# Kernel tuning notes

Measured on AMD Instinct MI355X. Metric: run time of the kernel, lower is better.

The kernel has to match this reference:

```python
import jax, jax.numpy as jnp
import numpy as np

NPOINT = 1024
NSAMPLE = 32
EPS = 1e-5


def setup_inputs() -> dict:
    key = jax.random.key(0)
    ks = jax.random.split(key, 8)
    B, N, D = 16, 4096, 64
    xyz = jax.random.normal(ks[0], (B, N, 3), dtype=jnp.float32)
    points = jax.random.normal(ks[1], (B, N, D), dtype=jnp.float32)

    def mk(k, o, i):
        return (jax.random.normal(k, (o, i), dtype=jnp.float32) * 0.05,
                jnp.zeros((o,), jnp.float32),   # conv bias
                jnp.ones((o,), jnp.float32),    # bn gamma
                jnp.zeros((o,), jnp.float32))   # bn beta

    W0, b0, g0, be0 = mk(ks[2], 64, 67)
    W1, b1, g1, be1 = mk(ks[3], 64, 64)
    W2, b2, g2, be2 = mk(ks[4], 128, 64)
    return dict(xyz=xyz, points=points,
                W0=W0, b0=b0, g0=g0, be0=be0,
                W1=W1, b1=b1, g1=g1, be1=be1,
                W2=W2, b2=b2, g2=g2, be2=be2)


def _fps(xyz, npoint):
    # Sequential farthest point sampling. xyz: [B,N,3] -> idx [B,npoint] int32.
    B, N, _ = xyz.shape
    bidx = jnp.arange(B)

    def step(carry, _):
        distance, farthest = carry
        centroid = xyz[bidx, farthest][:, None, :]          # [B,1,3]
        d = jnp.sum((xyz - centroid) ** 2, -1)              # [B,N]
        distance = jnp.minimum(distance, d)
        new_far = jnp.argmax(distance, -1).astype(jnp.int32)
        return (distance, new_far), farthest

    init = (jnp.full((B, N), jnp.inf, dtype=xyz.dtype),
            jnp.full((B,), N // 2, dtype=jnp.int32))
    _, cents = jax.lax.scan(step, init, None, length=npoint)
    return cents.T                                          # [B, npoint]


def _gather(p, idx):
    # p: [B,N,C], idx: [B,...] -> [B,...,C]
    return jax.vmap(lambda a, i: a[i])(p, idx)


def reference(xyz, points, W0, b0, g0, be0, W1, b1, g1, be1, W2, b2, g2, be2):
    B, N, _ = xyz.shape
    fps_idx = _fps(xyz, NPOINT)                             # [B,M]
    new_xyz = _gather(xyz, fps_idx)                         # [B,M,3]

    # squared distances [B,M,N], then k smallest neighbors
    d = (jnp.sum(new_xyz ** 2, -1)[:, :, None]
         + jnp.sum(xyz ** 2, -1)[:, None, :]
         - 2.0 * jnp.einsum('bmc,bnc->bmn', new_xyz, xyz))
    _, idx = jax.lax.top_k(-d, NSAMPLE)                     # [B,M,K]

    grouped_xyz = _gather(xyz, idx)                         # [B,M,K,3]
    rel = grouped_xyz - new_xyz[:, :, None, :]
    grouped_feat = _gather(points, idx)                     # [B,M,K,D]
    g = jnp.concatenate([rel, grouped_feat], axis=-1)       # [B,M,K,3+D]

    # 1x1 conv + BatchNorm2d (training-mode batch stats) + ReLU
    for W, b, gm, bt in ((W0, b0, g0, be0), (W1, b1, g1, be1), (W2, b2, g2, be2)):
        x = jnp.einsum('bmkc,oc->bmko', g, W) + b
        mu = x.mean((0, 1, 2))
        var = x.var((0, 1, 2))
        g = jax.nn.relu(gm * (x - mu) * jax.lax.rsqrt(var + EPS) + bt)

    new_points = g.max(axis=2)                              # [B,M,C_out]
    return new_xyz, new_points, fps_idx
```

## Files before the change

### kernel.cpp

```cpp
#include <hip/hip_runtime.h>
#include <math.h>

#define B_ 16
#define N_ 4096
#define D_ 64
#define M_ 1024
#define K_ 32
#define RTOT (B_*M_*K_)
#define EPSF 1e-5f

#define WT0B_OFF  0
#define WT1B_OFF  3072
#define WT2B_OFF  5120
#define ST_OFF    9216
#define BN_OFF    9728
#define NXW_OFF   10240
#define KIDX_OFF  59392
#define PK_OFF    583680
#define Y0B_OFF   2680832
#define PTS4_OFF  Y0B_OFF
#define Y1B_OFF   19458048
#define SB0_OFF   36235264
#define SB1_OFF   (SB0_OFF + 8192)
#define SB2_OFF   (SB1_OFF + 8192)
#define WS_FAST_BYTES ((unsigned long long)(SB2_OFF + 16384) * 4ull)

typedef __attribute__((ext_vector_type(8))) short bf16x8;
typedef __attribute__((ext_vector_type(4))) float f32x4;

__device__ inline unsigned bf16u(float x) {
    unsigned u = __float_as_uint(x);
    return (u + 0x7FFFu + ((u >> 16) & 1u)) >> 16;
}
__device__ inline float ubf(unsigned short h) {
    return __uint_as_float(((unsigned)h) << 16);
}

__global__ void prep_kernel(const float* __restrict__ W0, const float* __restrict__ W1,
                            const float* __restrict__ W2, float* __restrict__ ws,
                            int zero_sb) {
    int tid = threadIdx.x;
    if (blockIdx.x > 0) {
        if (zero_sb) {
            float* sb = ws + SB0_OFF + (blockIdx.x - 1) * 2048;
            for (int i = tid; i < 2048; i += 256) sb[i] = 0.f;
        }
        return;
    }
    unsigned short* wt0b = (unsigned short*)(ws + WT0B_OFF);
    unsigned short* wt1b = (unsigned short*)(ws + WT1B_OFF);
    unsigned short* wt2b = (unsigned short*)(ws + WT2B_OFF);
    float* st = ws + ST_OFF;
    for (int i = tid; i < 512; i += 256) st[i] = 0.f;
    for (int i = tid; i < 64*96; i += 256) {
        int o = i / 96, k = i - o*96;
        float w = 0.f;
        if (k < 64)      w = W0[o*67 + 3 + k];
        else if (k < 67) w = W0[o*67 + (k - 64)];
        wt0b[i] = (unsigned short)bf16u(w);
    }
    for (int i = tid; i < 64*64; i += 256)  wt1b[i] = (unsigned short)bf16u(W1[i]);
    for (int i = tid; i < 128*64; i += 256) wt2b[i] = (unsigned short)bf16u(W2[i]);
}

__global__ __launch_bounds__(256) void fps_kernel(const float* __restrict__ xyz,
                                                  float* __restrict__ out_newxyz,
                                                  float* __restrict__ out_fpsidx,
                                                  float* __restrict__ ws_newxyz,
                                                  float4* __restrict__ pts4g) {
#pragma clang fp contract(off)
    __shared__ float4 pts[N_];
    __shared__ int selidx[M_];
    __shared__ __align__(32) unsigned long long red[2][4];
    const int b = blockIdx.x;
    const int tid = threadIdx.x;
    const int lane = tid & 63, wave = tid >> 6;
    const float* xb = xyz + (size_t)b * N_ * 3;
    for (int i = tid; i < N_; i += 256) {
        float x = xb[i*3+0], y = xb[i*3+1], z = xb[i*3+2];
        pts[i] = make_float4(x, y, z, 0.f);
        if (pts4g) {
            float pp = x*x + y*y; pp = pp + z*z;
            pts4g[b*N_ + i] = make_float4(x, y, z, pp);
        }
    }
    __syncthreads();
    float px[16], py[16], pz[16], dist[16];
#pragma unroll
    for (int j = 0; j < 16; ++j) {
        float4 p = pts[(tid << 4) + j];
        px[j] = p.x; py[j] = p.y; pz[j] = p.z;
        dist[j] = 3.4e38f;
    }
    int cur = N_/2;
    for (int t = 0; t < M_; ++t) {
        if (tid == (t & 255)) selidx[t] = cur;
        if (t == M_-1) break;
        float4 c4 = pts[cur];
        float cx = c4.x, cy = c4.y, cz = c4.z;
        float bm0 = -1.f, bm1 = -1.f, bm2 = -1.f, bm3 = -1.f;
        int bj0 = 0, bj1 = 4, bj2 = 8, bj3 = 12;
#pragma unroll
        for (int j = 0; j < 4; ++j) {
            {
                float dx = px[j]-cx, dy = py[j]-cy, dz = pz[j]-cz;
                float a = dx*dx, b2 = dy*dy, c2 = dz*dz;
                float d = (a + b2) + c2;
                float nd = fminf(dist[j], d); dist[j] = nd;
                bool bt = nd > bm0; bm0 = bt ? nd : bm0; bj0 = bt ? j : bj0;
            }
            {
                int k = j + 4;
                float dx = px[k]-cx, dy = py[k]-cy, dz = pz[k]-cz;
                float a = dx*dx, b2 = dy*dy, c2 = dz*dz;
                float d = (a + b2) + c2;
                float nd = fminf(dist[k], d); dist[k] = nd;
                bool bt = nd > bm1; bm1 = bt ? nd : bm1; bj1 = bt ? k : bj1;
            }
            {
                int k = j + 8;
                float dx = px[k]-cx, dy = py[k]-cy, dz = pz[k]-cz;
                float a = dx*dx, b2 = dy*dy, c2 = dz*dz;
                float d = (a + b2) + c2;
                float nd = fminf(dist[k], d); dist[k] = nd;
                bool bt = nd > bm2; bm2 = bt ? nd : bm2; bj2 = bt ? k : bj2;
            }
            {
                int k = j + 12;
                float dx = px[k]-cx, dy = py[k]-cy, dz = pz[k]-cz;
                float a = dx*dx, b2 = dy*dy, c2 = dz*dz;
                float d = (a + b2) + c2;
                float nd = fminf(dist[k], d); dist[k] = nd;
                bool bt = nd > bm3; bm3 = bt ? nd : bm3; bj3 = bt ? k : bj3;
            }
        }
        float bv = bm0; int bj = bj0;
        if (bm1 > bv) { bv = bm1; bj = bj1; }
        if (bm2 > bv) { bv = bm2; bj = bj2; }
        if (bm3 > bv) { bv = bm3; bj = bj3; }
        unsigned mybits = __float_as_uint(bv);
        unsigned vr = mybits;
        { unsigned o = (unsigned)__builtin_amdgcn_update_dpp((int)vr,(int)vr,0x121,0xF,0xF,false); if (o > vr) vr = o; }
        { unsigned o = (unsigned)__builtin_amdgcn_update_dpp((int)vr,(int)vr,0x122,0xF,0xF,false); if (o > vr) vr = o; }
        { unsigned o = (unsigned)__builtin_amdgcn_update_dpp((int)vr,(int)vr,0x124,0xF,0xF,false); if (o > vr) vr = o; }
        { unsigned o = (unsigned)__builtin_amdgcn_update_dpp((int)vr,(int)vr,0x128,0xF,0xF,false); if (o > vr) vr = o; }
        unsigned r0 = (unsigned)__builtin_amdgcn_readlane((int)vr, 0);
        unsigned r1 = (unsigned)__builtin_amdgcn_readlane((int)vr, 16);
        unsigned r2 = (unsigned)__builtin_amdgcn_readlane((int)vr, 32);
        unsigned r3 = (unsigned)__builtin_amdgcn_readlane((int)vr, 48);
        unsigned m01 = (r0 > r1) ? r0 : r1;
        unsigned m23 = (r2 > r3) ? r2 : r3;
        unsigned vmax = (m01 > m23) ? m01 : m23;
        unsigned long long mask = __ballot(mybits == vmax);
        int wl = (int)__builtin_ctzll(mask);
        int gidx = (tid << 4) + bj;
        int sel = __builtin_amdgcn_readlane(gidx, wl);
        unsigned long long key = ((unsigned long long)vmax << 32) | (unsigned)(~sel);
        int buf = t & 1;
        if (lane == 0) red[buf][wave] = key;
        __syncthreads();
        unsigned long long k0 = red[buf][0], k1 = red[buf][1];
        unsigned long long k2 = red[buf][2], k3 = red[buf][3];
        unsigned long long km01 = (k0 > k1) ? k0 : k1;
        unsigned long long km23 = (k2 > k3) ? k2 : k3;
        unsigned long long km   = (km01 > km23) ? km01 : km23;
        cur = (int)((~(unsigned)km) & (N_-1));
    }
    __syncthreads();
    for (int i = tid; i < M_; i += 256) {
        int c = selidx[i];
        out_fpsidx[b*M_ + i] = (float)c;
        float4 p = pts[c];
        size_t o3 = (size_t)(b*M_ + i)*3;
        out_newxyz[o3+0] = p.x; out_newxyz[o3+1] = p.y; out_newxyz[o3+2] = p.z;
        ws_newxyz[o3+0] = p.x;  ws_newxyz[o3+1] = p.y;  ws_newxyz[o3+2] = p.z;
    }
}

__global__ __launch_bounds__(256) void knn_kernel4(const float4* __restrict__ pts4,
                                                   const float* __restrict__ ws_newxyz,
                                                   int* __restrict__ knn_idx) {
#pragma clang fp contract(off)
    const int lane = threadIdx.x & 63;
    const int q = blockIdx.x * 4 + (threadIdx.x >> 6);
    const int b = q >> 10;
    const float4* pb = pts4 + (size_t)b * N_;
    float qx = ws_newxyz[q*3+0], qy = ws_newxyz[q*3+1], qz = ws_newxyz[q*3+2];
    float qq = qx*qx + qy*qy; qq = qq + qz*qz;
    float val[64];
    float m1 = 3.4e38f, m2 = 3.4e38f; int k1 = 0, k2 = 0;
#pragma unroll
    for (int k = 0; k < 64; ++k) {
        float4 p = pb[(k<<6) + lane];
        float dot = qx*p.x + qy*p.y; dot = dot + qz*p.z;
        float d = (qq + p.w) - 2.0f*dot;
        val[k] = d;
        bool lt1 = d < m1, lt2 = d < m2;
        k2 = lt1 ? k1 : (lt2 ? k : k2);
        m2 = fminf(fmaxf(d, m1), m2);
        k1 = lt1 ? k : k1;
        m1 = fminf(d, m1);
    }
    unsigned long long consumed = 0ull;
    bool has2 = true;
    unsigned int myOut = 0;
    for (int r = 0; r < 32; ++r) {
        unsigned int u = __float_as_uint(m1);
        u = (u & 0x80000000u) ? ~u : (u | 0x80000000u);
        unsigned long long pk = ((unsigned long long)u << 32) | (unsigned)(lane + (k1<<6));
#pragma unroll
        for (int off = 32; off > 0; off >>= 1) {
            unsigned long long o = __shfl_xor(pk, off);
            pk = (o < pk) ? o : pk;
        }
        unsigned g = (unsigned)pk;
        if (lane == r) myOut = g;
        if (lane == (int)(g & 63u)) {
            consumed |= (1ull << k1);
            if (has2) { m1 = m2; k1 = k2; has2 = false; }
            else {
                m1 = 3.4e38f; k1 = 0;
#pragma unroll
                for (int k = 0; k < 64; ++k) {
                    bool ok = !((consumed >> k) & 1ull) && (val[k] < m1);
                    m1 = ok ? val[k] : m1;
                    k1 = ok ? k : k1;
                }
            }
        }
    }
    if (lane < 32) knn_idx[q*32 + lane] = (int)myOut;
}

__global__ __launch_bounds__(256) void knn_kernel(const float* __restrict__ xyz,
                                                  const float* __restrict__ ws_newxyz,
                                                  int* __restrict__ knn_idx) {
#pragma clang fp contract(off)
    const int lane = threadIdx.x & 63;
    const int q = blockIdx.x * 4 + (threadIdx.x >> 6);
    const int b = q >> 10;
    const float* xb = xyz + (size_t)b * N_ * 3;
    float qx = ws_newxyz[q*3+0], qy = ws_newxyz[q*3+1], qz = ws_newxyz[q*3+2];
    float qq = qx*qx + qy*qy; qq = qq + qz*qz;
    float val[64];
    float m1 = 3.4e38f, m2 = 3.4e38f; int k1 = 0, k2 = 0;
#pragma unroll
    for (int k = 0; k < 64; ++k) {
        int n = (k<<6) + lane;
        float x = xb[n*3+0], y = xb[n*3+1], z = xb[n*3+2];
        float pp = x*x + y*y; pp = pp + z*z;
        float dot = qx*x + qy*y; dot = dot + qz*z;
        float d = (qq + pp) - 2.0f*dot;
        val[k] = d;
        if (d < m1)      { m2 = m1; k2 = k1; m1 = d; k1 = k; }
        else if (d < m2) { m2 = d; k2 = k; }
    }
    unsigned long long consumed = 0ull;
    bool has2 = true;
    unsigned int myOut = 0;
    for (int r = 0; r < 32; ++r) {
        unsigned int u = __float_as_uint(m1);
        u = (u & 0x80000000u) ? ~u : (u | 0x80000000u);
        unsigned long long pk = ((unsigned long long)u << 32) | (unsigned)(lane + (k1<<6));
#pragma unroll
        for (int off = 32; off > 0; off >>= 1) {
            unsigned long long o = __shfl_xor(pk, off);
            pk = (o < pk) ? o : pk;
        }
        unsigned g = (unsigned)pk;
        if (lane == r) myOut = g;
        if (lane == (int)(g & 63u)) {
            consumed |= (1ull << k1);
            if (has2) { m1 = m2; k1 = k2; has2 = false; }
            else {
                m1 = 3.4e38f; k1 = 0;
#pragma unroll
                for (int k = 0; k < 64; ++k) {
                    bool ok = !((consumed >> k) & 1ull) && (val[k] < m1);
                    m1 = ok ? val[k] : m1;
                    k1 = ok ? k : k1;
                }
            }
        }
    }
    if (lane < 32) knn_idx[q*32 + lane] = (int)myOut;
}

__global__ __launch_bounds__(256) void pass0_kernel(
    const float* __restrict__ xyz, const float* __restrict__ points,
    const float* __restrict__ nxw, const int* __restrict__ kidx,
    const unsigned short* __restrict__ wt0b, const float* __restrict__ cb0,
    float* __restrict__ sb,
    unsigned short* __restrict__ y0b)
{
    __shared__ __align__(16) unsigned short XsB[64*104];
    __shared__ __align__(16) unsigned short W0B[64*104];
    __shared__ int sidx[64];
    __shared__ float sAcc[64], qAcc[64];
    const int tid = threadIdx.x;
    const int r0 = blockIdx.x * 64;
    const int lane = tid & 63, wv = tid >> 6;
    const int mrow = lane & 15, quad = lane >> 4;

    if (tid < 64) { sidx[tid] = kidx[r0 + tid]; sAcc[tid] = 0.f; qAcc[tid] = 0.f; }
    {
        const uint4* s = (const uint4*)wt0b;
        for (int i = tid; i < 768; i += 256) {
            int r = i / 12, ch = i - r*12;
            *(uint4*)(W0B + r*104 + ch*8) = s[i];
        }
    }
    __syncthreads();

    {
        int row = tid >> 2, q4 = tid & 3;
        int gr = r0 + row;
        int qq = gr >> 5, bb = qq >> 10;
        int n = sidx[row];
        const float4* src = (const float4*)(points + ((size_t)(bb*N_ + n))*64 + q4*16);
        float4 f0 = src[0], f1 = src[1], f2 = src[2], f3 = src[3];
        uint4 u0, u1;
        u0.x = bf16u(f0.x) | (bf16u(f0.y) << 16);
        u0.y = bf16u(f0.z) | (bf16u(f0.w) << 16);
        u0.z = bf16u(f1.x) | (bf16u(f1.y) << 16);
        u0.w = bf16u(f1.z) | (bf16u(f1.w) << 16);
        u1.x = bf16u(f2.x) | (bf16u(f2.y) << 16);
        u1.y = bf16u(f2.z) | (bf16u(f2.w) << 16);
        u1.z = bf16u(f3.x) | (bf16u(f3.y) << 16);
        u1.w = bf16u(f3.z) | (bf16u(f3.w) << 16);
        *(uint4*)(XsB + row*104 + q4*16)     = u0;
        *(uint4*)(XsB + row*104 + q4*16 + 8) = u1;
        uint4 z;
        if (q4 == 0) {
            float rx = xyz[((size_t)(bb*N_ + n))*3 + 0] - nxw[qq*3 + 0];
            float ry = xyz[((size_t)(bb*N_ + n))*3 + 1] - nxw[qq*3 + 1];
            float rz = xyz[((size_t)(bb*N_ + n))*3 + 2] - nxw[qq*3 + 2];
            z.x = bf16u(rx) | (bf16u(ry) << 16);
            z.y = bf16u(rz);
            z.z = 0; z.w = 0;
        } else { z.x = 0; z.y = 0; z.z = 0; z.w = 0; }
        *(uint4*)(XsB + row*104 + 64 + q4*8) = z;
    }
    __syncthreads();

    const int arow = wv*16 + mrow;
    f32x4 acc0[4];
#pragma unroll
    for (int ct = 0; ct < 4; ++ct) {
        float bv = cb0[ct*16 + mrow];
        acc0[ct] = (f32x4){bv, bv, bv, bv};
    }
#pragma unroll
    for (int kk = 0; kk < 96; kk += 32) {
        bf16x8 a = *(const bf16x8*)(XsB + arow*104 + kk + quad*8);
#pragma unroll
        for (int ct = 0; ct < 4; ++ct) {
            bf16x8 b = *(const bf16x8*)(W0B + (ct*16 + mrow)*104 + kk + quad*8);
            acc0[ct] = __builtin_amdgcn_mfma_f32_16x16x32_bf16(a, b, acc0[ct], 0, 0, 0);
        }
    }
#pragma unroll
    for (int ct = 0; ct < 4; ++ct) {
        f32x4 v = acc0[ct];
        float s = (v.x + v.y) + (v.z + v.w);
        float q = (v.x*v.x + v.y*v.y) + (v.z*v.z + v.w*v.w);
        atomicAdd(&sAcc[ct*16 + mrow], s);
        atomicAdd(&qAcc[ct*16 + mrow], q);
    }
    __syncthreads();
    unsigned short* STG = W0B;
    const int rbase = wv*16 + quad*4;
#pragma unroll
    for (int ct = 0; ct < 4; ++ct) {
        int col = ct*16 + mrow;
        f32x4 v = acc0[ct];
        STG[(rbase+0)*72 + col] = (unsigned short)bf16u(v.x);
        STG[(rbase+1)*72 + col] = (unsigned short)bf16u(v.y);
        STG[(rbase+2)*72 + col] = (unsigned short)bf16u(v.z);
        STG[(rbase+3)*72 + col] = (unsigned short)bf16u(v.w);
    }
    __syncthreads();
    for (int i = tid; i < 512; i += 256) {
        int r = i >> 3, c8 = i & 7;
        *(uint4*)(y0b + (size_t)(r0 + r)*64 + c8*8) = *(const uint4*)(STG + r*72 + c8*8);
    }
    int bk = blockIdx.x & 63;
    if (tid < 64) {
        atomicAdd(sb + bk*64 + tid, sAcc[tid]);
        atomicAdd(sb + 4096 + bk*64 + tid, qAcc[tid]);
    }
}

__global__ __launch_bounds__(256) void pass1_kernel(
    const unsigned short* __restrict__ y0b, const unsigned short* __restrict__ wt1b,
    const float* __restrict__ cb1, const float* __restrict__ bnab0,
    float* __restrict__ sb,
    unsigned short* __restrict__ y1b)
{
    __shared__ __align__(16) unsigned short W1B[64*72];
    __shared__ __align__(16) unsigned short STG[64*72];
    __shared__ float sAcc[64], qAcc[64];
    const int tid = threadIdx.x;
    const int r0 = blockIdx.x * 64;
    const int lane = tid & 63, wv = tid >> 6;
    const int mrow = lane & 15, quad = lane >> 4;

    {
        const uint4* s = (const uint4*)wt1b;
        for (int i = tid; i < 512; i += 256) {
            int r = i >> 3, ch = i & 7;
            *(uint4*)(W1B + r*72 + ch*8) = s[i];
        }
    }
    if (tid < 64) { sAcc[tid] = 0.f; qAcc[tid] = 0.f; }

    const int gr = r0 + wv*16 + mrow;
    bf16x8 raw0 = *(const bf16x8*)(y0b + (size_t)gr*64 + quad*8);
    bf16x8 raw1 = *(const bf16x8*)(y0b + (size_t)gr*64 + 32 + quad*8);
    bf16x8 a0, a1;
    {
        const float* A = bnab0 + quad*8;
        const float* S = bnab0 + 64 + quad*8;
#pragma unroll
        for (int j = 0; j < 8; ++j) {
            float f = ubf((unsigned short)raw0[j]);
            a0[j] = (short)bf16u(fmaxf(fmaf(A[j], f, S[j]), 0.f));
        }
        const float* A2 = bnab0 + 32 + quad*8;
        const float* S2 = bnab0 + 96 + quad*8;
#pragma unroll
        for (int j = 0; j < 8; ++j) {
            float f = ubf((unsigned short)raw1[j]);
            a1[j] = (short)bf16u(fmaxf(fmaf(A2[j], f, S2[j]), 0.f));
        }
    }
    __syncthreads();

    f32x4 acc[4];
#pragma unroll
    for (int ct = 0; ct < 4; ++ct) {
        float bv = cb1[ct*16 + mrow];
        acc[ct] = (f32x4){bv, bv, bv, bv};
    }
#pragma unroll
    for (int ct = 0; ct < 4; ++ct) {
        bf16x8 b0 = *(const bf16x8*)(W1B + (ct*16 + mrow)*72 + quad*8);
        bf16x8 b1 = *(const bf16x8*)(W1B + (ct*16 + mrow)*72 + 32 + quad*8);
        acc[ct] = __builtin_amdgcn_mfma_f32_16x16x32_bf16(a0, b0, acc[ct], 0, 0, 0);
        acc[ct] = __builtin_amdgcn_mfma_f32_16x16x32_bf16(a1, b1, acc[ct], 0, 0, 0);
    }
#pragma unroll
    for (int ct = 0; ct < 4; ++ct) {
        f32x4 v = acc[ct];
        float s = (v.x + v.y) + (v.z + v.w);
        float q = (v.x*v.x + v.y*v.y) + (v.z*v.z + v.w*v.w);
        atomicAdd(&sAcc[ct*16 + mrow], s);
        atomicAdd(&qAcc[ct*16 + mrow], q);
    }
    const int rbase = wv*16 + quad*4;
#pragma unroll
    for (int ct = 0; ct < 4; ++ct) {
        int col = ct*16 + mrow;
        f32x4 v = acc[ct];
        STG[(rbase+0)*72 + col] = (unsigned short)bf16u(v.x);
        STG[(rbase+1)*72 + col] = (unsigned short)bf16u(v.y);
        STG[(rbase+2)*72 + col] = (unsigned short)bf16u(v.z);
        STG[(rbase+3)*72 + col] = (unsigned short)bf16u(v.w);
    }
    __syncthreads();
    for (int i = tid; i < 512; i += 256) {
        int r = i >> 3, c8 = i & 7;
        *(uint4*)(y1b + (size_t)(r0 + r)*64 + c8*8) = *(const uint4*)(STG + r*72 + c8*8);
    }
    int bk = blockIdx.x & 63;
    if (tid < 64) {
        atomicAdd(sb + bk*64 + tid, sAcc[tid]);
        atomicAdd(sb + 4096 + bk*64 + tid, qAcc[tid]);
    }
}

__global__ __launch_bounds__(256) void pass2_kernel(
    const unsigned short* __restrict__ y1b, const unsigned short* __restrict__ wt2b,
    const float* __restrict__ cb2, const float* __restrict__ bnab1,
    float* __restrict__ sb,
    unsigned int* __restrict__ packed)
{
    __shared__ __align__(16) unsigned short W2B[128*72];
    __shared__ float sAcc[128], qAcc[128];
    __shared__ float mxs[4*128], mns[4*128];
    const int tid = threadIdx.x;
    const int r0 = blockIdx.x * 64;
    const int lane = tid & 63, wv = tid >> 6;
    const int mrow = lane & 15, quad = lane >> 4;

    {
        const uint4* s = (const uint4*)wt2b;
        for (int i = tid; i < 1024; i += 256) {
            int r = i >> 3, ch = i & 7;
            *(uint4*)(W2B + r*72 + ch*8) = s[i];
        }
    }
    if (tid < 128) { sAcc[tid] = 0.f; qAcc[tid] = 0.f; }

    const int gr = r0 + wv*16 + mrow;
    bf16x8 raw0 = *(const bf16x8*)(y1b + (size_t)gr*64 + quad*8);
    bf16x8 raw1 = *(const bf16x8*)(y1b + (size_t)gr*64 + 32 + quad*8);
    bf16x8 a0, a1;
    {
        const float* A = bnab1 + quad*8;
        const float* S = bnab1 + 64 + quad*8;
#pragma unroll
        for (int j = 0; j < 8; ++j) {
            float f = ubf((unsigned short)raw0[j]);
            a0[j] = (short)bf16u(fmaxf(fmaf(A[j], f, S[j]), 0.f));
        }
        const float* A2 = bnab1 + 32 + quad*8;
        const float* S2 = bnab1 + 96 + quad*8;
#pragma unroll
        for (int j = 0; j < 8; ++j) {
            float f = ubf((unsigned short)raw1[j]);
            a1[j] = (short)bf16u(fmaxf(fmaf(A2[j], f, S2[j]), 0.f));
        }
    }
    __syncthreads();

    f32x4 acc[8];
#pragma unroll
    for (int ct = 0; ct < 8; ++ct) {
        float bv = cb2[ct*16 + mrow];
        acc[ct] = (f32x4){bv, bv, bv, bv};
    }
#pragma unroll
    for (int ct = 0; ct < 8; ++ct) {
        bf16x8 b0 = *(const bf16x8*)(W2B + (ct*16 + mrow)*72 + quad*8);
        bf16x8 b1 = *(const bf16x8*)(W2B + (ct*16 + mrow)*72 + 32 + quad*8);
        acc[ct] = __builtin_amdgcn_mfma_f32_16x16x32_bf16(a0, b0, acc[ct], 0, 0, 0);
        acc[ct] = __builtin_amdgcn_mfma_f32_16x16x32_bf16(a1, b1, acc[ct], 0, 0, 0);
    }
#pragma unroll
    for (int ct = 0; ct < 8; ++ct) {
        f32x4 v = acc[ct];
        float s = (v.x + v.y) + (v.z + v.w);
        float q = (v.x*v.x + v.y*v.y) + (v.z*v.z + v.w*v.w);
        atomicAdd(&sAcc[ct*16 + mrow], s);
        atomicAdd(&qAcc[ct*16 + mrow], q);
    }
#pragma unroll
    for (int ct = 0; ct < 8; ++ct) {
        f32x4 v = acc[ct];
        float mx = fmaxf(fmaxf(v.x, v.y), fmaxf(v.z, v.w));
        float mn = fminf(fminf(v.x, v.y), fminf(v.z, v.w));
        { float o = __shfl_xor(mx, 16); mx = fmaxf(mx, o); }
        { float o = __shfl_xor(mn, 16); mn = fminf(mn, o); }
        { float o = __shfl_xor(mx, 32); mx = fmaxf(mx, o); }
        { float o = __shfl_xor(mn, 32); mn = fminf(mn, o); }
        if (quad == 0) {
            mxs[wv*128 + ct*16 + mrow] = mx;
            mns[wv*128 + ct*16 + mrow] = mn;
        }
    }
    __syncthreads();
    {
        int g = tid >> 7, c = tid & 127;
        float mx = fmaxf(mxs[(2*g)*128 + c], mxs[(2*g+1)*128 + c]);
        float mn = fminf(mns[(2*g)*128 + c], mns[(2*g+1)*128 + c]);
        packed[(size_t)(blockIdx.x*2 + g)*128 + c] = (bf16u(mx) << 16) | bf16u(mn);
    }
    int bk = blockIdx.x & 63;
    if (tid < 128) {
        atomicAdd(sb + bk*128 + tid, sAcc[tid]);
        atomicAdd(sb + 8192 + bk*128 + tid, qAcc[tid]);
    }
}

template<int DEPTH>
__global__ __launch_bounds__(256) void mlp_pass(
    const float* __restrict__ xyz, const float* __restrict__ points,
    const float* __restrict__ nxw, const int* __restrict__ kidx,
    const unsigned short* __restrict__ wt0b, const unsigned short* __restrict__ wt1b,
    const unsigned short* __restrict__ wt2b,
    const float* __restrict__ cb0, const float* __restrict__ cb1,
    const float* __restrict__ cb2,
    const float* __restrict__ bnab0, const float* __restrict__ bnab1,
    float* __restrict__ statS, float* __restrict__ statQ,
    unsigned int* __restrict__ packed)
{
    __shared__ __align__(16) unsigned short XsB[64*104];
    __shared__ __align__(16) unsigned short W0B[64*104];
    __shared__ __align__(16) unsigned short W1B[(DEPTH>=2) ? 64*72 : 8];
    __shared__ __align__(16) unsigned short W2B[(DEPTH==3) ? 128*72 : 8];
    __shared__ __align__(16) unsigned short Gb [(DEPTH>=2) ? 64*72 : 8];
    __shared__ float sAcc[128], qAcc[128];
    __shared__ float mxs[(DEPTH==3) ? 4*128 : 1];
    __shared__ float mns[(DEPTH==3) ? 4*128 : 1];

    const int tid = threadIdx.x;
    const int r0 = blockIdx.x * 64;
    const int lane = tid & 63, wv = tid >> 6;
    const int mrow = lane & 15, quad = lane >> 4;

    {
        const uint4* s = (const uint4*)wt0b;
        for (int i = tid; i < 768; i += 256) {
            int r = i / 12, ch = i - r*12;
            *(uint4*)(W0B + r*104 + ch*8) = s[i];
        }
    }
    if constexpr (DEPTH >= 2) {
        const uint4* s = (const uint4*)wt1b;
        for (int i = tid; i < 512; i += 256) {
            int r = i >> 3, ch = i & 7;
            *(uint4*)(W1B + r*72 + ch*8) = s[i];
        }
    }
    if constexpr (DEPTH == 3) {
        const uint4* s = (const uint4*)wt2b;
        for (int i = tid; i < 1024; i += 256) {
            int r = i >> 3, ch = i & 7;
            *(uint4*)(W2B + r*72 + ch*8) = s[i];
        }
    }
    if (tid < 128) { sAcc[tid] = 0.f; qAcc[tid] = 0.f; }

    for (int i = tid; i < 64*96; i += 256) {
        int r = i / 96, c = i - r*96;
        int gr = r0 + r;
        int q = gr >> 5;
        int n = kidx[gr];
        int bb = q >> 10;
        float v = 0.f;
        if (c < 64)      v = points[((size_t)(bb*N_ + n))*64 + c];
        else if (c < 67) v = xyz[((size_t)(bb*N_ + n))*3 + (c-64)] - nxw[q*3 + (c-64)];
        XsB[r*104 + c] = (unsigned short)bf16u(v);
    }
    __syncthreads();

    const int arow = wv*16 + mrow;
    f32x4 acc0[4];
#pragma unroll
    for (int ct = 0; ct < 4; ++ct) {
        float bv = cb0[ct*16 + mrow];
        acc0[ct] = (f32x4){bv, bv, bv, bv};
    }
#pragma unroll
    for (int kk = 0; kk < 96; kk += 32) {
        bf16x8 a = *(const bf16x8*)(XsB + arow*104 + kk + quad*8);
#pragma unroll
        for (int ct = 0; ct < 4; ++ct) {
            bf16x8 b = *(const bf16x8*)(W0B + (ct*16 + mrow)*104 + kk + quad*8);
            acc0[ct] = __builtin_amdgcn_mfma_f32_16x16x32_bf16(a, b, acc0[ct], 0, 0, 0);
        }
    }

    if constexpr (DEPTH == 1) {
#pragma unroll
        for (int ct = 0; ct < 4; ++ct) {
            f32x4 v = acc0[ct];
            float s = (v.x + v.y) + (v.z + v.w);
            float q = (v.x*v.x + v.y*v.y) + (v.z*v.z + v.w*v.w);
            atomicAdd(&sAcc[ct*16 + mrow], s);
            atomicAdd(&qAcc[ct*16 + mrow], q);
        }
        __syncthreads();
        if (tid < 64) { atomicAdd(statS + tid, sAcc[tid]); atomicAdd(statQ + tid, qAcc[tid]); }
        return;
    } else {
        const int rbase = wv*16 + quad*4;
#pragma unroll
        for (int ct = 0; ct < 4; ++ct) {
            int col = ct*16 + mrow;
            float a = bnab0[col], sh = bnab0[64 + col];
            f32x4 v = acc0[ct];
            Gb[(rbase+0)*72 + col] = (unsigned short)bf16u(fmaxf(fmaf(a, v.x, sh), 0.f));
            Gb[(rbase+1)*72 + col] = (unsigned short)bf16u(fmaxf(fmaf(a, v.y, sh), 0.f));
            Gb[(rbase+2)*72 + col] = (unsigned short)bf16u(fmaxf(fmaf(a, v.z, sh), 0.f));
            Gb[(rbase+3)*72 + col] = (unsigned short)bf16u(fmaxf(fmaf(a, v.w, sh), 0.f));
        }
        f32x4 acc1[4];
#pragma unroll
        for (int ct = 0; ct < 4; ++ct) {
            float bv = cb1[ct*16 + mrow];
            acc1[ct] = (f32x4){bv, bv, bv, bv};
        }
#pragma unroll
        for (int kk = 0; kk < 64; kk += 32) {
            bf16x8 a = *(const bf16x8*)(Gb + arow*72 + kk + quad*8);
#pragma unroll
            for (int ct = 0; ct < 4; ++ct) {
                bf16x8 b = *(const bf16x8*)(W1B + (ct*16 + mrow)*72 + kk + quad*8);
                acc1[ct] = __builtin_amdgcn_mfma_f32_16x16x32_bf16(a, b, acc1[ct], 0, 0, 0);
            }
        }
        if constexpr (DEPTH == 2) {
#pragma unroll
            for (int ct = 0; ct < 4; ++ct) {
                f32x4 v = acc1[ct];
                float s = (v.x + v.y) + (v.z + v.w);
                float q = (v.x*v.x + v.y*v.y) + (v.z*v.z + v.w*v.w);
                atomicAdd(&sAcc[ct*16 + mrow], s);
                atomicAdd(&qAcc[ct*16 + mrow], q);
            }
            __syncthreads();
            if (tid < 64) { atomicAdd(statS + tid, sAcc[tid]); atomicAdd(statQ + tid, qAcc[tid]); }
            return;
        } else {
#pragma unroll
            for (int ct = 0; ct < 4; ++ct) {
                int col = ct*16 + mrow;
                float a = bnab1[col], sh = bnab1[64 + col];
                f32x4 v = acc1[ct];
                Gb[(rbase+0)*72 + col] = (unsigned short)bf16u(fmaxf(fmaf(a, v.x, sh), 0.f));
                Gb[(rbase+1)*72 + col] = (unsigned short)bf16u(fmaxf(fmaf(a, v.y, sh), 0.f));
                Gb[(rbase+2)*72 + col] = (unsigned short)bf16u(fmaxf(fmaf(a, v.z, sh), 0.f));
                Gb[(rbase+3)*72 + col] = (unsigned short)bf16u(fmaxf(fmaf(a, v.w, sh), 0.f));
            }
            f32x4 acc2[8];
#pragma unroll
            for (int ct = 0; ct < 8; ++ct) {
                float bv = cb2[ct*16 + mrow];
                acc2[ct] = (f32x4){bv, bv, bv, bv};
            }
#pragma unroll
            for (int kk = 0; kk < 64; kk += 32) {
                bf16x8 a = *(const bf16x8*)(Gb + arow*72 + kk + quad*8);
#pragma unroll
                for (int ct = 0; ct < 8; ++ct) {
                    bf16x8 b = *(const bf16x8*)(W2B + (ct*16 + mrow)*72 + kk + quad*8);
                    acc2[ct] = __builtin_amdgcn_mfma_f32_16x16x32_bf16(a, b, acc2[ct], 0, 0, 0);
                }
            }
#pragma unroll
            for (int ct = 0; ct < 8; ++ct) {
                f32x4 v = acc2[ct];
                float s = (v.x + v.y) + (v.z + v.w);
                float q = (v.x*v.x + v.y*v.y) + (v.z*v.z + v.w*v.w);
                atomicAdd(&sAcc[ct*16 + mrow], s);
                atomicAdd(&qAcc[ct*16 + mrow], q);
            }
#pragma unroll
            for (int ct = 0; ct < 8; ++ct) {
                f32x4 v = acc2[ct];
                float mx = fmaxf(fmaxf(v.x, v.y), fmaxf(v.z, v.w));
                float mn = fminf(fminf(v.x, v.y), fminf(v.z, v.w));
                { float o = __shfl_xor(mx, 16); mx = fmaxf(mx, o); }
                { float o = __shfl_xor(mn, 16); mn = fminf(mn, o); }
                { float o = __shfl_xor(mx, 32); mx = fmaxf(mx, o); }
                { float o = __shfl_xor(mn, 32); mn = fminf(mn, o); }
                if (quad == 0) {
                    mxs[wv*128 + ct*16 + mrow] = mx;
                    mns[wv*128 + ct*16 + mrow] = mn;
                }
            }
            __syncthreads();
            {
                int g = tid >> 7, c = tid & 127;
                float mx = fmaxf(mxs[(2*g)*128 + c], mxs[(2*g+1)*128 + c]);
                float mn = fminf(mns[(2*g)*128 + c], mns[(2*g+1)*128 + c]);
                packed[(size_t)(blockIdx.x*2 + g)*128 + c] = (bf16u(mx) << 16) | bf16u(mn);
            }
            if (tid < 128) { atomicAdd(statS + tid, sAcc[tid]); atomicAdd(statQ + tid, qAcc[tid]); }
        }
    }
}

template<int COUT>
__global__ void bn_finalize(const float* __restrict__ stat_s, const float* __restrict__ stat_q,
                            const float* __restrict__ gamma, const float* __restrict__ beta,
                            float* __restrict__ bnab) {
    int c = threadIdx.x;
    if (c < COUT) {
        const float inv_n = 1.f / (float)RTOT;
        float mu  = stat_s[c] * inv_n;
        float var = stat_q[c] * inv_n - mu*mu;
        float inv = 1.f / sqrtf(var + EPSF);
        float a = gamma[c] * inv;
        bnab[c] = a;
        bnab[COUT + c] = beta[c] - mu * a;
    }
}

template<int COUT>
__global__ __launch_bounds__(256) void bn_finalize_bk(const float* __restrict__ sb,
                               const float* __restrict__ gamma, const float* __restrict__ beta,
                               float* __restrict__ bnab) {
    __shared__ float ps[256], pq[256];
    const int tid = threadIdx.x;
    const int c = tid & (COUT - 1);
    const int g = tid / COUT;
    const int G = 256 / COUT;
    const int per = 64 / G;
    float s = 0.f, q = 0.f;
    for (int k = g*per; k < (g+1)*per; ++k) {
        s += sb[k*COUT + c];
        q += sb[64*COUT + k*COUT + c];
    }
    ps[tid] = s; pq[tid] = q;
    __syncthreads();
    if (tid < COUT) {
        for (int g2 = 1; g2 < G; ++g2) { s += ps[g2*COUT + tid]; q += pq[g2*COUT + tid]; }
        const float inv_n = 1.f / (float)RTOT;
        float mu  = s * inv_n;
        float var = q * inv_n - mu*mu;
        float inv = 1.f / sqrtf(var + EPSF);
        float a = gamma[tid] * inv;
        bnab[tid] = a;
        bnab[COUT + tid] = beta[tid] - mu * a;
    }
}

__global__ __launch_bounds__(256) void final_out(const unsigned int* __restrict__ packed,
                                                 const float* __restrict__ bnab2,
                                                 float* __restrict__ out_np) {
    int idx = blockIdx.x*256 + threadIdx.x;
    int c = idx & 127;
    float a = bnab2[c], sh = bnab2[128 + c];
    unsigned p = packed[idx];
    float mx = __uint_as_float(p & 0xFFFF0000u);
    float mn = __uint_as_float(p << 16);
    float x = (a >= 0.f) ? mx : mn;
    out_np[idx] = fmaxf(fmaf(a, x, sh), 0.f);
}

extern "C" void kernel_launch(void* const* d_in, const int* in_sizes, int n_in,
                              void* d_out, int out_size, void* d_ws, size_t ws_size,
                              hipStream_t stream) {
    const float* xyz    = (const float*)d_in[0];
    const float* points = (const float*)d_in[1];
    const float* W0 = (const float*)d_in[2];
    const float* b0 = (const float*)d_in[3];
    const float* g0 = (const float*)d_in[4];
    const float* be0= (const float*)d_in[5];
    const float* W1 = (const float*)d_in[6];
    const float* b1 = (const float*)d_in[7];
    const float* g1 = (const float*)d_in[8];
    const float* be1= (const float*)d_in[9];
    const float* W2 = (const float*)d_in[10];
    const float* b2 = (const float*)d_in[11];
    const float* g2 = (const float*)d_in[12];
    const float* be2= (const float*)d_in[13];

    float* ws  = (float*)d_ws;
    float* out = (float*)d_out;
    float* out_newxyz = out;
    float* out_np     = out + 49152;
    float* out_fpsidx = out + 49152 + 2097152;

    unsigned short* wt0b = (unsigned short*)(ws + WT0B_OFF);
    unsigned short* wt1b = (unsigned short*)(ws + WT1B_OFF);
    unsigned short* wt2b = (unsigned short*)(ws + WT2B_OFF);
    float* s0 = ws + ST_OFF;        float* q0 = s0 + 64;
    float* s1 = q0 + 64;            float* q1 = s1 + 64;
    float* s2 = q1 + 64;            float* q2 = s2 + 128;
    float* bnab0 = ws + BN_OFF;     float* bnab1 = bnab0 + 128;  float* bnab2 = bnab1 + 128;
    float* nxw   = ws + NXW_OFF;
    int*   kidx  = (int*)(ws + KIDX_OFF);
    unsigned int* packed = (unsigned int*)(ws + PK_OFF);
    unsigned short* y0b = (unsigned short*)(ws + Y0B_OFF);
    unsigned short* y1b = (unsigned short*)(ws + Y1B_OFF);
    float4* pts4 = (float4*)(ws + PTS4_OFF);
    float* sb0 = ws + SB0_OFF;
    float* sb1 = ws + SB1_OFF;
    float* sb2 = ws + SB2_OFF;

    int fast = (ws_size >= WS_FAST_BYTES) ? 1 : 0;

    prep_kernel<<<17, 256, 0, stream>>>(W0, W1, W2, ws, fast);
    fps_kernel<<<B_, 256, 0, stream>>>(xyz, out_newxyz, out_fpsidx, nxw,
                                       fast ? pts4 : nullptr);
    if (fast)
        knn_kernel4<<<(B_*M_)/4, 256, 0, stream>>>(pts4, nxw, kidx);
    else
        knn_kernel<<<(B_*M_)/4, 256, 0, stream>>>(xyz, nxw, kidx);

    if (fast) {
        pass0_kernel<<<RTOT/64, 256, 0, stream>>>(xyz, points, nxw, kidx, wt0b, b0, sb0, y0b);
        bn_finalize_bk<64><<<1, 256, 0, stream>>>(sb0, g0, be0, bnab0);
        pass1_kernel<<<RTOT/64, 256, 0, stream>>>(y0b, wt1b, b1, bnab0, sb1, y1b);
        bn_finalize_bk<64><<<1, 256, 0, stream>>>(sb1, g1, be1, bnab1);
        pass2_kernel<<<RTOT/64, 256, 0, stream>>>(y1b, wt2b, b2, bnab1, sb2, packed);
        bn_finalize_bk<128><<<1, 256, 0, stream>>>(sb2, g2, be2, bnab2);
    } else {
        mlp_pass<1><<<RTOT/64, 256, 0, stream>>>(xyz, points, nxw, kidx, wt0b, wt1b, wt2b,
            b0, b1, b2, nullptr, nullptr, s0, q0, nullptr);
        bn_finalize<64><<<1, 64, 0, stream>>>(s0, q0, g0, be0, bnab0);
        mlp_pass<2><<<RTOT/64, 256, 0, stream>>>(xyz, points, nxw, kidx, wt0b, wt1b, wt2b,
            b0, b1, b2, bnab0, nullptr, s1, q1, nullptr);
        bn_finalize<64><<<1, 64, 0, stream>>>(s1, q1, g1, be1, bnab1);
        mlp_pass<3><<<RTOT/64, 256, 0, stream>>>(xyz, points, nxw, kidx, wt0b, wt1b, wt2b,
            b0, b1, b2, bnab0, bnab1, s2, q2, packed);
        bn_finalize<128><<<1, 128, 0, stream>>>(s2, q2, g2, be2, bnab2);
    }

    final_out<<<(B_*M_*128)/256, 256, 0, stream>>>(packed, bnab2, out_np);
}
```

Measured before the change: 1.309 ms.

## Recompute layer-1 in pass2, pre-convert points to bf16, DPP reduction in kNN

pass1 now only accumulates BatchNorm statistics and no longer writes y1 to global memory. pass2 recomputes layer-1 from y0 using W1 and then feeds the result to layer-2, trading extra MFMA work for skipping the y1 write and read. The points tensor is converted once to bf16 in extra prep blocks, so pass0 gathers half the bytes with no per-row conversion. The kNN argmin reduction uses DPP row_ror steps for the intra-row stages instead of shuffles.

```diff
diff --git a/kernel.cpp b/kernel.cpp
--- a/kernel.cpp
+++ b/kernel.cpp
@@ -19,7 +19,7 @@
 #define PK_OFF    583680
 #define Y0B_OFF   2680832
 #define PTS4_OFF  Y0B_OFF
-#define Y1B_OFF   19458048
+#define PBF_OFF   19458048
 #define SB0_OFF   36235264
 #define SB1_OFF   (SB0_OFF + 8192)
 #define SB2_OFF   (SB1_OFF + 8192)
@@ -36,13 +36,35 @@
     return __uint_as_float(((unsigned)h) << 16);
 }
 
+#define ROR_MIN(kvar, CTRL) do {                                                   \
+    unsigned _lo = (unsigned)(kvar), _hi = (unsigned)((kvar) >> 32);               \
+    unsigned _rl = (unsigned)__builtin_amdgcn_update_dpp((int)_lo, (int)_lo, CTRL, 0xF, 0xF, false); \
+    unsigned _rh = (unsigned)__builtin_amdgcn_update_dpp((int)_hi, (int)_hi, CTRL, 0xF, 0xF, false); \
+    unsigned long long _o = ((unsigned long long)_rh << 32) | _rl;                 \
+    if (_o < (kvar)) (kvar) = _o;                                                  \
+} while (0)
+
 __global__ void prep_kernel(const float* __restrict__ W0, const float* __restrict__ W1,
-                            const float* __restrict__ W2, float* __restrict__ ws,
-                            int zero_sb) {
+                            const float* __restrict__ W2, const float* __restrict__ points,
+                            float* __restrict__ ws, int fast) {
     int tid = threadIdx.x;
-    if (blockIdx.x > 0) {
-        if (zero_sb) {
-            float* sb = ws + SB0_OFF + (blockIdx.x - 1) * 2048;
+    int bx = blockIdx.x;
+    if (bx >= 17) {
+        unsigned short* pbf = (unsigned short*)(ws + PBF_OFF);
+        size_t base = (size_t)(bx - 17) * 2048 + (size_t)tid * 8;
+        const float4* s = (const float4*)(points + base);
+        float4 f0 = s[0], f1 = s[1];
+        uint4 u;
+        u.x = bf16u(f0.x) | (bf16u(f0.y) << 16);
+        u.y = bf16u(f0.z) | (bf16u(f0.w) << 16);
+        u.z = bf16u(f1.x) | (bf16u(f1.y) << 16);
+        u.w = bf16u(f1.z) | (bf16u(f1.w) << 16);
+        *(uint4*)(pbf + base) = u;
+        return;
+    }
+    if (bx > 0) {
+        if (fast) {
+            float* sb = ws + SB0_OFF + (bx - 1) * 2048;
             for (int i = tid; i < 2048; i += 256) sb[i] = 0.f;
         }
         return;
@@ -208,11 +230,12 @@
         unsigned int u = __float_as_uint(m1);
         u = (u & 0x80000000u) ? ~u : (u | 0x80000000u);
         unsigned long long pk = ((unsigned long long)u << 32) | (unsigned)(lane + (k1<<6));
-#pragma unroll
-        for (int off = 32; off > 0; off >>= 1) {
-            unsigned long long o = __shfl_xor(pk, off);
-            pk = (o < pk) ? o : pk;
-        }
+        ROR_MIN(pk, 0x121);
+        ROR_MIN(pk, 0x122);
+        ROR_MIN(pk, 0x124);
+        ROR_MIN(pk, 0x128);
+        { unsigned long long o = __shfl_xor(pk, 16); if (o < pk) pk = o; }
+        { unsigned long long o = __shfl_xor(pk, 32); if (o < pk) pk = o; }
         unsigned g = (unsigned)pk;
         if (lane == r) myOut = g;
         if (lane == (int)(g & 63u)) {
@@ -287,7 +310,7 @@
 }
 
 __global__ __launch_bounds__(256) void pass0_kernel(
-    const float* __restrict__ xyz, const float* __restrict__ points,
+    const float* __restrict__ xyz, const unsigned short* __restrict__ pbf,
     const float* __restrict__ nxw, const int* __restrict__ kidx,
     const unsigned short* __restrict__ wt0b, const float* __restrict__ cb0,
     float* __restrict__ sb,
@@ -317,19 +340,9 @@
         int gr = r0 + row;
         int qq = gr >> 5, bb = qq >> 10;
         int n = sidx[row];
-        const float4* src = (const float4*)(points + ((size_t)(bb*N_ + n))*64 + q4*16);
-        float4 f0 = src[0], f1 = src[1], f2 = src[2], f3 = src[3];
-        uint4 u0, u1;
-        u0.x = bf16u(f0.x) | (bf16u(f0.y) << 16);
-        u0.y = bf16u(f0.z) | (bf16u(f0.w) << 16);
-        u0.z = bf16u(f1.x) | (bf16u(f1.y) << 16);
-        u0.w = bf16u(f1.z) | (bf16u(f1.w) << 16);
-        u1.x = bf16u(f2.x) | (bf16u(f2.y) << 16);
-        u1.y = bf16u(f2.z) | (bf16u(f2.w) << 16);
-        u1.z = bf16u(f3.x) | (bf16u(f3.y) << 16);
-        u1.w = bf16u(f3.z) | (bf16u(f3.w) << 16);
-        *(uint4*)(XsB + row*104 + q4*16)     = u0;
-        *(uint4*)(XsB + row*104 + q4*16 + 8) = u1;
+        const uint4* src = (const uint4*)(pbf + ((size_t)(bb*N_ + n))*64 + q4*16);
+        *(uint4*)(XsB + row*104 + q4*16)     = src[0];
+        *(uint4*)(XsB + row*104 + q4*16 + 8) = src[1];
         uint4 z;
         if (q4 == 0) {
             float rx = xyz[((size_t)(bb*N_ + n))*3 + 0] - nxw[qq*3 + 0];
@@ -394,11 +407,9 @@
 __global__ __launch_bounds__(256) void pass1_kernel(
     const unsigned short* __restrict__ y0b, const unsigned short* __restrict__ wt1b,
     const float* __restrict__ cb1, const float* __restrict__ bnab0,
-    float* __restrict__ sb,
-    unsigned short* __restrict__ y1b)
+    float* __restrict__ sb)
 {
     __shared__ __align__(16) unsigned short W1B[64*72];
-    __shared__ __align__(16) unsigned short STG[64*72];
     __shared__ float sAcc[64], qAcc[64];
     const int tid = threadIdx.x;
     const int r0 = blockIdx.x * 64;
@@ -457,21 +468,7 @@
         atomicAdd(&sAcc[ct*16 + mrow], s);
         atomicAdd(&qAcc[ct*16 + mrow], q);
     }
-    const int rbase = wv*16 + quad*4;
-#pragma unroll
-    for (int ct = 0; ct < 4; ++ct) {
-        int col = ct*16 + mrow;
-        f32x4 v = acc[ct];
-        STG[(rbase+0)*72 + col] = (unsigned short)bf16u(v.x);
-        STG[(rbase+1)*72 + col] = (unsigned short)bf16u(v.y);
-        STG[(rbase+2)*72 + col] = (unsigned short)bf16u(v.z);
-        STG[(rbase+3)*72 + col] = (unsigned short)bf16u(v.w);
-    }
-    __syncthreads();
-    for (int i = tid; i < 512; i += 256) {
-        int r = i >> 3, c8 = i & 7;
-        *(uint4*)(y1b + (size_t)(r0 + r)*64 + c8*8) = *(const uint4*)(STG + r*72 + c8*8);
-    }
+    __syncthreads();
     int bk = blockIdx.x & 63;
     if (tid < 64) {
         atomicAdd(sb + bk*64 + tid, sAcc[tid]);
@@ -480,12 +477,16 @@
 }
 
 __global__ __launch_bounds__(256) void pass2_kernel(
-    const unsigned short* __restrict__ y1b, const unsigned short* __restrict__ wt2b,
-    const float* __restrict__ cb2, const float* __restrict__ bnab1,
+    const unsigned short* __restrict__ y0b,
+    const unsigned short* __restrict__ wt1b, const unsigned short* __restrict__ wt2b,
+    const float* __restrict__ cb1, const float* __restrict__ cb2,
+    const float* __restrict__ bnab0, const float* __restrict__ bnab1,
     float* __restrict__ sb,
     unsigned int* __restrict__ packed)
 {
+    __shared__ __align__(16) unsigned short W1B[64*72];
     __shared__ __align__(16) unsigned short W2B[128*72];
+    __shared__ __align__(16) unsigned short Gb[64*72];
     __shared__ float sAcc[128], qAcc[128];
     __shared__ float mxs[4*128], mns[4*128];
     const int tid = threadIdx.x;
@@ -494,6 +495,13 @@
     const int mrow = lane & 15, quad = lane >> 4;
 
     {
+        const uint4* s = (const uint4*)wt1b;
+        for (int i = tid; i < 512; i += 256) {
+            int r = i >> 3, ch = i & 7;
+            *(uint4*)(W1B + r*72 + ch*8) = s[i];
+        }
+    }
+    {
         const uint4* s = (const uint4*)wt2b;
         for (int i = tid; i < 1024; i += 256) {
             int r = i >> 3, ch = i & 7;
@@ -503,19 +511,19 @@
     if (tid < 128) { sAcc[tid] = 0.f; qAcc[tid] = 0.f; }
 
     const int gr = r0 + wv*16 + mrow;
-    bf16x8 raw0 = *(const bf16x8*)(y1b + (size_t)gr*64 + quad*8);
-    bf16x8 raw1 = *(const bf16x8*)(y1b + (size_t)gr*64 + 32 + quad*8);
+    bf16x8 raw0 = *(const bf16x8*)(y0b + (size_t)gr*64 + quad*8);
+    bf16x8 raw1 = *(const bf16x8*)(y0b + (size_t)gr*64 + 32 + quad*8);
     bf16x8 a0, a1;
     {
-        const float* A = bnab1 + quad*8;
-        const float* S = bnab1 + 64 + quad*8;
+        const float* A = bnab0 + quad*8;
+        const float* S = bnab0 + 64 + quad*8;
 #pragma unroll
         for (int j = 0; j < 8; ++j) {
             float f = ubf((unsigned short)raw0[j]);
             a0[j] = (short)bf16u(fmaxf(fmaf(A[j], f, S[j]), 0.f));
         }
-        const float* A2 = bnab1 + 32 + quad*8;
-        const float* S2 = bnab1 + 96 + quad*8;
+        const float* A2 = bnab0 + 32 + quad*8;
+        const float* S2 = bnab0 + 96 + quad*8;
 #pragma unroll
         for (int j = 0; j < 8; ++j) {
             float f = ubf((unsigned short)raw1[j]);
@@ -524,6 +532,32 @@
     }
     __syncthreads();
 
+    f32x4 acc1[4];
+#pragma unroll
+    for (int ct = 0; ct < 4; ++ct) {
+        float bv = cb1[ct*16 + mrow];
+        acc1[ct] = (f32x4){bv, bv, bv, bv};
+    }
+#pragma unroll
+    for (int ct = 0; ct < 4; ++ct) {
+        bf16x8 b0 = *(const bf16x8*)(W1B + (ct*16 + mrow)*72 + quad*8);
+        bf16x8 b1 = *(const bf16x8*)(W1B + (ct*16 + mrow)*72 + 32 + quad*8);
+        acc1[ct] = __builtin_amdgcn_mfma_f32_16x16x32_bf16(a0, b0, acc1[ct], 0, 0, 0);
+        acc1[ct] = __builtin_amdgcn_mfma_f32_16x16x32_bf16(a1, b1, acc1[ct], 0, 0, 0);
+    }
+    const int rbase = wv*16 + quad*4;
+#pragma unroll
+    for (int ct = 0; ct < 4; ++ct) {
+        int col = ct*16 + mrow;
+        float a = bnab1[col], sh = bnab1[64 + col];
+        f32x4 v = acc1[ct];
+        Gb[(rbase+0)*72 + col] = (unsigned short)bf16u(fmaxf(fmaf(a, v.x, sh), 0.f));
+        Gb[(rbase+1)*72 + col] = (unsigned short)bf16u(fmaxf(fmaf(a, v.y, sh), 0.f));
+        Gb[(rbase+2)*72 + col] = (unsigned short)bf16u(fmaxf(fmaf(a, v.z, sh), 0.f));
+        Gb[(rbase+3)*72 + col] = (unsigned short)bf16u(fmaxf(fmaf(a, v.w, sh), 0.f));
+    }
+
+    const int arow = wv*16 + mrow;
     f32x4 acc[8];
 #pragma unroll
     for (int ct = 0; ct < 8; ++ct) {
@@ -531,11 +565,13 @@
         acc[ct] = (f32x4){bv, bv, bv, bv};
     }
 #pragma unroll
-    for (int ct = 0; ct < 8; ++ct) {
-        bf16x8 b0 = *(const bf16x8*)(W2B + (ct*16 + mrow)*72 + quad*8);
-        bf16x8 b1 = *(const bf16x8*)(W2B + (ct*16 + mrow)*72 + 32 + quad*8);
-        acc[ct] = __builtin_amdgcn_mfma_f32_16x16x32_bf16(a0, b0, acc[ct], 0, 0, 0);
-        acc[ct] = __builtin_amdgcn_mfma_f32_16x16x32_bf16(a1, b1, acc[ct], 0, 0, 0);
+    for (int kk = 0; kk < 64; kk += 32) {
+        bf16x8 a = *(const bf16x8*)(Gb + arow*72 + kk + quad*8);
+#pragma unroll
+        for (int ct = 0; ct < 8; ++ct) {
+            bf16x8 b = *(const bf16x8*)(W2B + (ct*16 + mrow)*72 + kk + quad*8);
+            acc[ct] = __builtin_amdgcn_mfma_f32_16x16x32_bf16(a, b, acc[ct], 0, 0, 0);
+        }
     }
 #pragma unroll
     for (int ct = 0; ct < 8; ++ct) {
@@ -856,7 +892,7 @@
     int*   kidx  = (int*)(ws + KIDX_OFF);
     unsigned int* packed = (unsigned int*)(ws + PK_OFF);
     unsigned short* y0b = (unsigned short*)(ws + Y0B_OFF);
-    unsigned short* y1b = (unsigned short*)(ws + Y1B_OFF);
+    unsigned short* pbf = (unsigned short*)(ws + PBF_OFF);
     float4* pts4 = (float4*)(ws + PTS4_OFF);
     float* sb0 = ws + SB0_OFF;
     float* sb1 = ws + SB1_OFF;
@@ -864,7 +900,7 @@
 
     int fast = (ws_size >= WS_FAST_BYTES) ? 1 : 0;
 
-    prep_kernel<<<17, 256, 0, stream>>>(W0, W1, W2, ws, fast);
+    prep_kernel<<<fast ? (17 + 2048) : 17, 256, 0, stream>>>(W0, W1, W2, points, ws, fast);
     fps_kernel<<<B_, 256, 0, stream>>>(xyz, out_newxyz, out_fpsidx, nxw,
                                        fast ? pts4 : nullptr);
     if (fast)
@@ -873,11 +909,11 @@
         knn_kernel<<<(B_*M_)/4, 256, 0, stream>>>(xyz, nxw, kidx);
 
     if (fast) {
-        pass0_kernel<<<RTOT/64, 256, 0, stream>>>(xyz, points, nxw, kidx, wt0b, b0, sb0, y0b);
+        pass0_kernel<<<RTOT/64, 256, 0, stream>>>(xyz, pbf, nxw, kidx, wt0b, b0, sb0, y0b);
         bn_finalize_bk<64><<<1, 256, 0, stream>>>(sb0, g0, be0, bnab0);
-        pass1_kernel<<<RTOT/64, 256, 0, stream>>>(y0b, wt1b, b1, bnab0, sb1, y1b);
+        pass1_kernel<<<RTOT/64, 256, 0, stream>>>(y0b, wt1b, b1, bnab0, sb1);
         bn_finalize_bk<64><<<1, 256, 0, stream>>>(sb1, g1, be1, bnab1);
-        pass2_kernel<<<RTOT/64, 256, 0, stream>>>(y1b, wt2b, b2, bnab1, sb2, packed);
+        pass2_kernel<<<RTOT/64, 256, 0, stream>>>(y0b, wt1b, wt2b, b1, b2, bnab0, bnab1, sb2, packed);
         bn_finalize_bk<128><<<1, 256, 0, stream>>>(sb2, g2, be2, bnab2);
     } else {
         mlp_pass<1><<<RTOT/64, 256, 0, stream>>>(xyz, points, nxw, kidx, wt0b, wt1b, wt2b,
```

Result: no change. 1.309 ms (+0.0%).
